# Kernel optimization log

Hardware: AMD Instinct MI355X
Metric: run time of the kernel (lower is better)

The kernel has to match this reference:

```python
import jax, jax.numpy as jnp
import numpy as np

EPS = 1e-6          # module eps for denominator
KERNEL_EPS = 1e-4   # performer softmax_kernel numerical eps


def softmax_kernel(data, projection):
    # data: [n, l, h, e]; projection: [m, e] -> features [n, l, h, m]
    d = data.shape[-1]
    m = projection.shape[0]
    data_normalizer = d ** -0.25
    ratio = m ** -0.5
    data_dash = jnp.einsum('nlhe,me->nlhm', data * data_normalizer, projection)
    diag_data = (0.5 * (data_normalizer ** 2)) * jnp.sum(data * data, axis=-1, keepdims=True)
    # numerically stable exp with per-row max subtraction
    data_dash = ratio * (jnp.exp(data_dash - diag_data - jnp.max(data_dash, axis=-1, keepdims=True)) + KERNEL_EPS)
    return data_dash


def _gaussian_orthogonal_random_matrix(nb_rows, nb_cols, seed=0):
    rng = np.random.default_rng(seed)
    blocks = []
    for _ in range(int(np.ceil(nb_rows / nb_cols))):
        q, _ = np.linalg.qr(rng.standard_normal((nb_cols, nb_cols)))
        blocks.append(q.T)
    proj = np.concatenate(blocks, axis=0)[:nb_rows]
    # scaling=0: chi-distributed row multipliers
    multiplier = np.linalg.norm(rng.standard_normal((nb_rows, nb_cols)), axis=1)
    return (multiplier[:, None] * proj).astype(np.float32)


def setup_inputs() -> dict:
    n, l, h, e = 2, 2048, 8, 64
    nb_features = l  # module: nb_features = l when l >= e
    key = jax.random.key(0)
    kq, kk, kv = jax.random.split(key, 3)
    queries = jax.random.normal(kq, (n, l, h, e), jnp.float32)
    keys = jax.random.normal(kk, (n, l, h, e), jnp.float32)
    values = jax.random.normal(kv, (n, l, h, e), jnp.float32)
    projection = jnp.asarray(_gaussian_orthogonal_random_matrix(nb_features, e))
    return {"queries": queries, "keys": keys, "values": values, "projection": projection}


def reference(queries, keys, values, projection):
    # Performer linear attention, batched (bi=None) branch
    q = softmax_kernel(queries, projection)   # [n, l, h, m]
    k = softmax_kernel(keys, projection)      # [n, l, h, m]
    kv = jnp.einsum('nshm,nshe->nhem', k, values)              # [n, h, e, m]
    z = 1.0 / (jnp.einsum('nlhm,nhm->nlh', q, k.sum(axis=1)) + EPS)  # [n, l, h]
    v = jnp.einsum('nlhm,nhem,nlh->nlhe', q, kv, z)             # [n, l, h, e]
    return v
```

## Files before the change

kernel.cpp:

```cpp
#include <hip/hip_runtime.h>


#define LL 2048
#define HH 8
#define MM 2048
#define ROWSTR 512

#define NORMC 0.35355339059327373f
#define LOG2E 1.4426950408889634f
#define NORMC2 (NORMC * LOG2E)
#define RATIO 0.022097086912079608f
#define KEPS 1e-4f
#define REPS (RATIO * KEPS)
#define EPSD 1e-6f

#define KVSPLIT 2097152
#define RSPLIT 32768

typedef __attribute__((ext_vector_type(8))) short short8;
typedef __attribute__((ext_vector_type(16))) float f32x16;

#define MFMA32(a, b, c) __builtin_amdgcn_mfma_f32_32x32x16_bf16((a), (b), (c), 0, 0, 0)

__device__ __forceinline__ void wg_barrier_lds() {
    asm volatile("s_waitcnt lgkmcnt(0)" ::: "memory");
    __builtin_amdgcn_s_barrier();
    __builtin_amdgcn_sched_barrier(0);
}

__device__ __forceinline__ f32x16 zero16() {
    f32x16 v;
    #pragma unroll
    for (int i = 0; i < 16; ++i) v[i] = 0.f;
    return v;
}
__device__ __forceinline__ unsigned short f2bf(float f) {
    union { float f; unsigned int u; } v; v.f = f;
    unsigned int r = v.u + 0x7fffu + ((v.u >> 16) & 1u);
    return (unsigned short)(r >> 16);
}
__device__ __forceinline__ unsigned int pk2(float lo, float hi) {
    return __builtin_amdgcn_perm(__float_as_uint(hi), __float_as_uint(lo), 0x07060302u);
}
__device__ __forceinline__ float bf2f(unsigned short u) {
    union { unsigned int ui; float f; } v; v.ui = ((unsigned int)u) << 16; return v.f;
}

template <bool BF16>
__device__ __forceinline__ short8 row_load8(const void* src, size_t rowbase, int off) {
    if (BF16) {
        return *(const short8*)((const unsigned short*)src + rowbase + off);
    } else {
        const float* p = (const float*)src + rowbase + off;
        float4 f0 = ((const float4*)p)[0], f1 = ((const float4*)p)[1];
        union { unsigned int u[4]; short8 s; } v;
        v.u[0] = pk2(f0.x, f0.y); v.u[1] = pk2(f0.z, f0.w);
        v.u[2] = pk2(f1.x, f1.y); v.u[3] = pk2(f1.z, f1.w);
        return v.s;
    }
}

template <bool BF16>
__device__ __forceinline__ void tile_load(const void* src, size_t base, size_t rstride,
                                          int t, uint4& A, uint4& B) {
    const int row = t >> 2, c16 = (t & 3) * 16;
    if (BF16) {
        const unsigned short* p = (const unsigned short*)src + base + (size_t)row * rstride + c16;
        A = *(const uint4*)p;
        B = *(const uint4*)(p + 8);
    } else {
        const float* p = (const float*)src + base + (size_t)row * rstride + c16;
        float4 f0 = ((const float4*)p)[0], f1 = ((const float4*)p)[1];
        float4 f2 = ((const float4*)p)[2], f3 = ((const float4*)p)[3];
        A.x = pk2(f0.x, f0.y); A.y = pk2(f0.z, f0.w);
        A.z = pk2(f1.x, f1.y); A.w = pk2(f1.z, f1.w);
        B.x = pk2(f2.x, f2.y); B.y = pk2(f2.z, f2.w);
        B.z = pk2(f3.x, f3.y); B.w = pk2(f3.z, f3.w);
    }
}
__device__ __forceinline__ void tile_store72(unsigned short* D, int t, uint4 A, uint4 B) {
    const int row = t >> 2, c16 = (t & 3) * 16;
    *(uint4*)&D[row * 72 + c16] = A;
    *(uint4*)&D[row * 72 + c16 + 8] = B;
}

template <bool BF16>
__device__ __forceinline__ void vt_load(const void* V, size_t base, int t, uint4& A, uint4& B) {
    const int s0 = (t & 31) * 2, e0 = (t >> 5) * 8;
    if (BF16) {
        const unsigned short* p = (const unsigned short*)V + base + (size_t)s0 * ROWSTR + e0;
        A = *(const uint4*)p;
        B = *(const uint4*)(p + ROWSTR);
    } else {
        const float* p = (const float*)V + base + (size_t)s0 * ROWSTR + e0;
        float4 f0 = ((const float4*)p)[0], f1 = ((const float4*)p)[1];
        const float* q = p + ROWSTR;
        float4 g0 = ((const float4*)q)[0], g1 = ((const float4*)q)[1];
        A.x = pk2(f0.x, f0.y); A.y = pk2(f0.z, f0.w);
        A.z = pk2(f1.x, f1.y); A.w = pk2(f1.z, f1.w);
        B.x = pk2(g0.x, g0.y); B.y = pk2(g0.z, g0.w);
        B.z = pk2(g1.x, g1.y); B.w = pk2(g1.z, g1.w);
    }
}
__device__ __forceinline__ void vt_store72(unsigned short* VT, int t, uint4 A, uint4 B) {
    const int s0 = (t & 31) * 2, e0 = (t >> 5) * 8;
    const unsigned ua[4] = {A.x, A.y, A.z, A.w}, ub[4] = {B.x, B.y, B.z, B.w};
    #pragma unroll
    for (int i = 0; i < 4; ++i) {
        *(unsigned*)&VT[(e0 + 2 * i) * 72 + s0] = (ua[i] & 0xFFFFu) | (ub[i] << 16);
        *(unsigned*)&VT[(e0 + 2 * i + 1) * 72 + s0] = (ua[i] >> 16) | (ub[i] & 0xFFFF0000u);
    }
}

__device__ __forceinline__ short8 xfrag(const unsigned int pd[8], int cp, int hi) {
    const unsigned int s0 = hi ? pd[4 * cp + 0] : pd[4 * cp + 2];
    const unsigned int s1 = hi ? pd[4 * cp + 1] : pd[4 * cp + 3];
    const unsigned int r0 = (unsigned int)__shfl_xor((int)s0, 32);
    const unsigned int r1 = (unsigned int)__shfl_xor((int)s1, 32);
    union { unsigned int u[4]; short8 s; } v;
    v.u[0] = hi ? r0 : pd[4 * cp + 0];
    v.u[1] = hi ? r1 : pd[4 * cp + 1];
    v.u[2] = hi ? pd[4 * cp + 2] : r0;
    v.u[3] = hi ? pd[4 * cp + 3] : r1;
    return v.s;
}

__global__ void LinearAttention_15985868276494_detect(const unsigned short* __restrict__ P,
                                                      float* __restrict__ flag) {
    if (threadIdx.x == 0) {
        int sane = 1;
        #pragma unroll
        for (int i = 0; i < 16; ++i) {
            const unsigned e = (P[2 * i] >> 7) & 0xFF;
            if (e < 101 || e > 141) sane = 0;
        }
        *flag = sane ? 1.0f : 0.0f;
    }
}

template <bool BF16>
__device__ void stats_impl(const void* X, const void* P, float* cws, char* smem) {
    unsigned short* Ps = (unsigned short*)smem;
    float* red = (float*)(smem + 73728);
    const int t = threadIdx.x;
    const int w = t >> 6, ln = t & 31, hi = (t >> 5) & 1;
    const int mstrip = w & 1, r3 = (w >> 1) & 3, tsel = w >> 3;
    const int grp = w >> 2, tl = t & 255;
    const int row_base = blockIdx.x * 128;

    short8 xb[4];
    #pragma unroll
    for (int c = 0; c < 4; ++c)
        xb[c] = row_load8<BF16>(X, (size_t)(row_base + r3 * 32 + ln) * 64, 16 * c + 8 * hi);

    uint4 pA, pB;
    {
        uint4 a0, b0;
        tile_load<BF16>(P, (size_t)(grp * 64) * 64, 64, tl, a0, b0);
        tile_store72(Ps + grp * 4608, tl, a0, b0);
        tile_load<BF16>(P, (size_t)((4 + grp) * 64) * 64, 64, tl, pA, pB);
    }
    wg_barrier_lds();

    float rmax = -3e38f;
    for (int i = 0; i < 8; ++i) {
        const int cur = i & 1;
        unsigned short* Pq = Ps + cur * 18432;
        #pragma unroll
        for (int j = 0; j < 2; ++j) {
            unsigned short* Pc = Pq + (tsel * 2 + j) * 4608;
            f32x16 acc = zero16();
            #pragma unroll
            for (int c = 0; c < 4; ++c) {
                const short8 af = *(const short8*)&Pc[(32 * mstrip + ln) * 72 + 16 * c + 8 * hi];
                acc = MFMA32(af, xb[c], acc);
            }
            #pragma unroll
            for (int r = 0; r < 16; ++r) rmax = fmaxf(rmax, acc[r]);
            if (j == 0 && i + 1 < 8) {
                tile_store72(Ps + (cur ^ 1) * 18432 + grp * 4608, tl, pA, pB);
                if (i + 2 < 8)
                    tile_load<BF16>(P, (size_t)(((i + 2) * 4 + grp) * 64) * 64, 64, tl, pA, pB);
            }
        }
        wg_barrier_lds();
    }
    rmax = fmaxf(rmax, __shfl_xor(rmax, 32));
    if (hi == 0) red[w * 32 + ln] = rmax;
    float s2 = 0.f;
    if (mstrip == 0 && tsel == 0) {
        #pragma unroll
        for (int c = 0; c < 4; ++c) {
            union { short8 s; unsigned int u[4]; } uv; uv.s = xb[c];
            #pragma unroll
            for (int i2 = 0; i2 < 4; ++i2) {
                const float lo = bf2f((unsigned short)(uv.u[i2] & 0xFFFF));
                const float hv = bf2f((unsigned short)(uv.u[i2] >> 16));
                s2 = fmaf(lo, lo, s2); s2 = fmaf(hv, hv, s2);
            }
        }
        s2 += __shfl_xor(s2, 32);
    }
    wg_barrier_lds();
    if (mstrip == 0 && tsel == 0 && hi == 0) {
        const float rm = fmaxf(fmaxf(red[(r3 * 2) * 32 + ln], red[(r3 * 2 + 1) * 32 + ln]),
                               fmaxf(red[(8 + r3 * 2) * 32 + ln], red[(8 + r3 * 2 + 1) * 32 + ln]));
        const int rg = row_base + r3 * 32 + ln;
        const int n = rg >> 14, l = (rg >> 3) & 2047, h = rg & 7;
        cws[(size_t)((n << 3) | h) * LL + l] =
            (NORMC * rm + (0.5f * NORMC * NORMC) * s2) * LOG2E;
    }
}

__global__ __launch_bounds__(1024, 4) void LinearAttention_15985868276494_stats(
        const void* K, const void* Q, const void* P, const float* flag,
        float* c_k, float* c_q) {
    extern __shared__ char smem_st[];
    const void* X = (blockIdx.y == 0) ? K : Q;
    float* cws = (blockIdx.y == 0) ? c_k : c_q;
    if (*flag != 0.f) stats_impl<true>(X, P, cws, smem_st);
    else stats_impl<false>(X, P, cws, smem_st);
}

template <bool BF16>
__device__ void kv_impl(const void* K, const void* V, const void* P, const float* cws,
                        float* kvf01, float* ksum01, char* smem) {
    unsigned short* Ks = (unsigned short*)smem;
    unsigned short* VT = (unsigned short*)(smem + 18432);
    float* cks = (float*)(smem + 36864);

    const int t = threadIdx.x;
    const int w = t >> 6, ln = t & 31, hi = (t >> 5) & 1;
    const int mc = w;
    const int bid = blockIdx.x;
    const int xcd = bid & 7, rr = bid >> 3;
    const int gq = rr >> 3, mtb = rr & 7;
    const int g = gq * 8 + xcd;
    const int nh = g >> 2, sp = g & 3;
    const int n = nh >> 3, h = nh & 7;
    const size_t xbase = (size_t)n * (LL * ROWSTR) + (size_t)h * 64;
    const int st0 = sp * 8;
    const int mbase = mtb * 256;

    const bool stK = (t < 256);
    const int tl = t & 255;

    short8 pb[4];
    #pragma unroll
    for (int c = 0; c < 4; ++c)
        pb[c] = row_load8<BF16>(P, (size_t)(mbase + mc * 32 + ln) * 64, 16 * c + 8 * hi);

    uint4 kA, kB, vA, vB; float ckr = 0.f;
    if (stK) {
        tile_load<BF16>(K, xbase + (size_t)(st0 * 64) * ROWSTR, ROWSTR, tl, kA, kB);
        tile_store72(Ks, tl, kA, kB);
        tile_load<BF16>(K, xbase + (size_t)((st0 + 1) * 64) * ROWSTR, ROWSTR, tl, kA, kB);
    } else {
        vt_load<BF16>(V, xbase + (size_t)(st0 * 64) * ROWSTR, tl, vA, vB);
        vt_store72(VT, tl, vA, vB);
        vt_load<BF16>(V, xbase + (size_t)((st0 + 1) * 64) * ROWSTR, tl, vA, vB);
    }
    if (t < 64) {
        cks[t] = cws[(size_t)nh * LL + st0 * 64 + t];
        ckr = cws[(size_t)nh * LL + (st0 + 1) * 64 + t];
    }
    wg_barrier_lds();

    f32x16 akv0 = zero16(), akv1 = zero16();
    float ks = 0.f;

    for (int i = 0; i < 8; ++i) {
        const int cur = i & 1;
        unsigned short* Kc = Ks + cur * 4608;
        unsigned short* Vc = VT + cur * 4608;
        const float* cc = cks + cur * 64;
        #pragma unroll
        for (int ss = 0; ss < 2; ++ss) {
            f32x16 D = zero16();
            #pragma unroll
            for (int c = 0; c < 4; ++c) {
                const short8 af = *(const short8*)&Kc[(32 * ss + ln) * 72 + 16 * c + 8 * hi];
                D = MFMA32(af, pb[c], D);
            }
            if (ss == 0 && i + 1 < 8) {
                if (stK) tile_store72(Ks + (cur ^ 1) * 4608, tl, kA, kB);
                else vt_store72(VT + (cur ^ 1) * 4608, tl, vA, vB);
                if (t < 64) cks[(cur ^ 1) * 64 + t] = ckr;
                if (i + 2 < 8) {
                    const int st = st0 + i + 2;
                    if (stK) tile_load<BF16>(K, xbase + (size_t)(st * 64) * ROWSTR, ROWSTR, tl, kA, kB);
                    else vt_load<BF16>(V, xbase + (size_t)(st * 64) * ROWSTR, tl, vA, vB);
                    if (t < 64) ckr = cws[(size_t)nh * LL + st * 64 + t];
                }
            }
            unsigned int pd[8];
            #pragma unroll
            for (int gIdx = 0; gIdx < 4; ++gIdx) {
                const float4 c4 = *(const float4*)&cc[32 * ss + 8 * gIdx + 4 * hi];
                const float ca[4] = {c4.x, c4.y, c4.z, c4.w};
                float f[4];
                #pragma unroll
                for (int b = 0; b < 4; ++b) {
                    const float arg = fminf(fmaf(D[4 * gIdx + b], NORMC2, -ca[b]), 0.f);
                    f[b] = fmaf(__builtin_amdgcn_exp2f(arg), RATIO, REPS);
                }
                ks += (f[0] + f[1]) + (f[2] + f[3]);
                pd[2 * gIdx] = pk2(f[0], f[1]);
                pd[2 * gIdx + 1] = pk2(f[2], f[3]);
            }
            #pragma unroll
            for (int cp = 0; cp < 2; ++cp) {
                const short8 bf = xfrag(pd, cp, hi);
                const int scol = 32 * ss + 16 * cp + 8 * hi;
                const short8 v0 = *(const short8*)&Vc[ln * 72 + scol];
                const short8 v1 = *(const short8*)&Vc[(32 + ln) * 72 + scol];
                akv0 = MFMA32(v0, bf, akv0);
                akv1 = MFMA32(v1, bf, akv1);
            }
        }
        wg_barrier_lds();
    }
    {
        ks += __shfl_xor(ks, 32);
        const int m = mbase + mc * 32 + ln;
        if (hi == 0)
            ksum01[(size_t)sp * RSPLIT + (size_t)nh * MM + m] = ks;
        float* basep = kvf01 + (size_t)sp * KVSPLIT + (size_t)nh * (size_t)(64 * MM) + m;
        #pragma unroll
        for (int r = 0; r < 16; ++r) {
            const int e = (r & 3) + 8 * (r >> 2) + 4 * hi;
            basep[(size_t)e * MM] = akv0[r];
            basep[(size_t)(e + 32) * MM] = akv1[r];
        }
    }
}

__global__ __launch_bounds__(512, 4) void LinearAttention_15985868276494_kv(
        const void* K, const void* V, const void* P, const float* flag,
        const float* cws, float* kvf01, float* ksum01) {
    extern __shared__ char smem_kv[];
    if (*flag != 0.f) kv_impl<true>(K, V, P, cws, kvf01, ksum01, smem_kv);
    else kv_impl<false>(K, V, P, cws, kvf01, ksum01, smem_kv);
}

__global__ __launch_bounds__(256) void LinearAttention_15985868276494_reduce(
        const float* __restrict__ kvf01, const float* __restrict__ ksum01,
        unsigned short* __restrict__ kvT, float* __restrict__ ksumW) {
    const int gid = blockIdx.x * 256 + threadIdx.x;
    const size_t i4 = (size_t)gid * 4;
    const float4 a = *(const float4*)&kvf01[i4];
    const float4 b = *(const float4*)&kvf01[KVSPLIT + i4];
    const float4 c = *(const float4*)&kvf01[2 * (size_t)KVSPLIT + i4];
    const float4 d = *(const float4*)&kvf01[3 * (size_t)KVSPLIT + i4];
    uint2 o;
    o.x = (unsigned)f2bf(a.x + b.x + c.x + d.x) | ((unsigned)f2bf(a.y + b.y + c.y + d.y) << 16);
    o.y = (unsigned)f2bf(a.z + b.z + c.z + d.z) | ((unsigned)f2bf(a.w + b.w + c.w + d.w) << 16);
    *(uint2*)&kvT[i4] = o;
    if (blockIdx.x < 32) {
        const float4 e = *(const float4*)&ksum01[i4];
        const float4 f = *(const float4*)&ksum01[RSPLIT + i4];
        const float4 g = *(const float4*)&ksum01[2 * RSPLIT + i4];
        const float4 h = *(const float4*)&ksum01[3 * RSPLIT + i4];
        *(float4*)&ksumW[i4] = make_float4(e.x + f.x + g.x + h.x, e.y + f.y + g.y + h.y,
                                           e.z + f.z + g.z + h.z, e.w + f.w + g.w + h.w);
    }
}

template <bool BF16>
__device__ void out_impl(const void* Q, const void* P, const float* cqw,
                         const unsigned short* kvT, const float* ksum,
                         float* po, float* pad, char* smem) {
    unsigned short* Ps = (unsigned short*)smem;
    unsigned short* KVs = (unsigned short*)(smem + 18432);
    unsigned short* kss = (unsigned short*)(smem + 36864);
    float* fin = (float*)smem;

    const int t = threadIdx.x;
    const int w = t >> 6, ln = t & 31, hi = (t >> 5) & 1;
    const int lc = w;
    const int bid = blockIdx.x;
    const int xcd = bid & 7, rr = bid >> 3;
    const int gq = rr >> 3, lbb = rr & 7;
    const int g = gq * 8 + xcd;
    const int nh = g >> 2, sp = g & 3;
    const int n = nh >> 3, h = nh & 7;
    const size_t qbase = (size_t)n * (LL * ROWSTR) + (size_t)h * 64;
    const size_t kvbase = (size_t)nh * (size_t)(64 * MM);
    const int mt0 = sp * 8;
    const int lbase = lbb * 256;

    const bool stP = (t < 256);
    const int tl = t & 255;

    short8 qb[4];
    #pragma unroll
    for (int c = 0; c < 4; ++c)
        qb[c] = row_load8<BF16>(Q, qbase + (size_t)(lbase + lc * 32 + ln) * ROWSTR, 16 * c + 8 * hi);
    const float cq = cqw[(size_t)nh * LL + lbase + lc * 32 + ln];

    uint4 pA, pB, kA, kB; float ksr = 0.f;
    if (stP) {
        tile_load<BF16>(P, (size_t)(mt0 * 64) * 64, 64, tl, pA, pB);
        tile_store72(Ps, tl, pA, pB);
        tile_load<BF16>(P, (size_t)((mt0 + 1) * 64) * 64, 64, tl, pA, pB);
    } else {
        tile_load<true>(kvT, kvbase + mt0 * 64, MM, tl, kA, kB);
        tile_store72(KVs, tl, kA, kB);
        tile_load<true>(kvT, kvbase + (mt0 + 1) * 64, MM, tl, kA, kB);
    }
    if (t < 64) {
        kss[t] = f2bf(ksum[(size_t)nh * MM + mt0 * 64 + t]);
        ksr = ksum[(size_t)nh * MM + (mt0 + 1) * 64 + t];
    }
    wg_barrier_lds();

    f32x16 ao0 = zero16(), ao1 = zero16(), ad = zero16();

    for (int i = 0; i < 8; ++i) {
        const int cur = i & 1;
        unsigned short* Pc = Ps + cur * 4608;
        unsigned short* Kc = KVs + cur * 4608;
        const unsigned short* ksc = kss + cur * 64;
        #pragma unroll
        for (int ms = 0; ms < 2; ++ms) {
            f32x16 D = zero16();
            #pragma unroll
            for (int c = 0; c < 4; ++c) {
                const short8 af = *(const short8*)&Pc[(32 * ms + ln) * 72 + 16 * c + 8 * hi];
                D = MFMA32(af, qb[c], D);
            }
            if (ms == 0 && i + 1 < 8) {
                if (stP) tile_store72(Ps + (cur ^ 1) * 4608, tl, pA, pB);
                else tile_store72(KVs + (cur ^ 1) * 4608, tl, kA, kB);
                if (t < 64) kss[(cur ^ 1) * 64 + t] = f2bf(ksr);
                if (i + 2 < 8) {
                    if (stP) tile_load<BF16>(P, (size_t)((mt0 + i + 2) * 64) * 64, 64, tl, pA, pB);
                    else tile_load<true>(kvT, kvbase + (mt0 + i + 2) * 64, MM, tl, kA, kB);
                    if (t < 64) ksr = ksum[(size_t)nh * MM + (mt0 + i + 2) * 64 + t];
                }
            }
            unsigned int pd[8];
            #pragma unroll
            for (int gIdx = 0; gIdx < 4; ++gIdx) {
                float f[4];
                #pragma unroll
                for (int b = 0; b < 4; ++b) {
                    const float arg = fminf(fmaf(D[4 * gIdx + b], NORMC2, -cq), 0.f);
                    f[b] = fmaf(__builtin_amdgcn_exp2f(arg), RATIO, REPS);
                }
                pd[2 * gIdx] = pk2(f[0], f[1]);
                pd[2 * gIdx + 1] = pk2(f[2], f[3]);
            }
            #pragma unroll
            for (int cp = 0; cp < 2; ++cp) {
                const short8 bf = xfrag(pd, cp, hi);
                const int mcol = 32 * ms + 16 * cp + 8 * hi;
                const short8 a0 = *(const short8*)&Kc[ln * 72 + mcol];
                const short8 a1 = *(const short8*)&Kc[(32 + ln) * 72 + mcol];
                const short8 k8 = *(const short8*)&ksc[mcol];
                ao0 = MFMA32(a0, bf, ao0);
                ao1 = MFMA32(a1, bf, ao1);
                ad = MFMA32(k8, bf, ad);
            }
        }
        wg_barrier_lds();
    }
    #pragma unroll 1
    for (int e2 = 0; e2 < 2; ++e2) {
        if ((w >> 2) == e2) {
            const int slot = ((w & 3) * 64 + (t & 63)) * 33;
            #pragma unroll
            for (int r = 0; r < 16; ++r) fin[slot + r] = ao0[r];
            #pragma unroll
            for (int r = 0; r < 16; ++r) fin[slot + 16 + r] = ao1[r];
            fin[slot + 32] = ad[0];
        }
        wg_barrier_lds();
        {
            const int l128 = t >> 2, eg = t & 3;
            const int w2 = l128 >> 5, lane_l = l128 & 31;
            const float adt = fin[(w2 * 64 + lane_l) * 33 + 32];
            const int l = lbase + (e2 * 4 + w2) * 32 + lane_l;
            const size_t row = (size_t)(n * LL + l) * HH + h;
            if (eg == 0) pad[(size_t)sp * RSPLIT + row] = adt;
            float* dst = po + (size_t)sp * KVSPLIT + row * 64 + eg * 16;
            #pragma unroll
            for (int jq = 0; jq < 4; ++jq) {
                float o[4];
                #pragma unroll
                for (int b = 0; b < 4; ++b) {
                    const int e = eg * 16 + 4 * jq + b;
                    const int t16 = e >> 5, e5 = e & 31;
                    const int hi_s = (e5 >> 2) & 1;
                    const int reg = 16 * t16 + (e5 & 3) + 4 * (e5 >> 3);
                    const int lane_s = hi_s * 32 + lane_l;
                    o[b] = fin[(w2 * 64 + lane_s) * 33 + reg];
                }
                *(float4*)&dst[4 * jq] = make_float4(o[0], o[1], o[2], o[3]);
            }
        }
        wg_barrier_lds();
    }
}

__global__ __launch_bounds__(512, 4) void LinearAttention_15985868276494_out(
        const void* Q, const void* P, const float* flag, const float* cqw,
        const unsigned short* kvT, const float* ksum, float* po, float* pad) {
    extern __shared__ char smem_out[];
    if (*flag != 0.f) out_impl<true>(Q, P, cqw, kvT, ksum, po, pad, smem_out);
    else out_impl<false>(Q, P, cqw, kvT, ksum, po, pad, smem_out);
}

__global__ __launch_bounds__(256) void LinearAttention_15985868276494_out2(
        const float* __restrict__ po, const float* __restrict__ pad,
        const float* __restrict__ flag, void* __restrict__ outp) {
    const int gid = blockIdx.x * 256 + threadIdx.x;
    const int row = gid >> 2, eg = gid & 3;
    const float adt = pad[row] + pad[RSPLIT + row]
                    + pad[2 * RSPLIT + row] + pad[3 * RSPLIT + row];
    const float z = 1.0f / (adt + EPSD);
    const size_t base = (size_t)row * 64 + eg * 16;
    float vals[16];
    #pragma unroll
    for (int q4 = 0; q4 < 4; ++q4) {
        const float4 a = *(const float4*)&po[base + 4 * q4];
        const float4 b = *(const float4*)&po[KVSPLIT + base + 4 * q4];
        const float4 c = *(const float4*)&po[2 * (size_t)KVSPLIT + base + 4 * q4];
        const float4 d = *(const float4*)&po[3 * (size_t)KVSPLIT + base + 4 * q4];
        vals[4 * q4 + 0] = (a.x + b.x + c.x + d.x) * z;
        vals[4 * q4 + 1] = (a.y + b.y + c.y + d.y) * z;
        vals[4 * q4 + 2] = (a.z + b.z + c.z + d.z) * z;
        vals[4 * q4 + 3] = (a.w + b.w + c.w + d.w) * z;
    }
    if (*flag != 0.f) {
        uint4 o0, o1;
        o0.x = (unsigned)f2bf(vals[0]) | ((unsigned)f2bf(vals[1]) << 16);
        o0.y = (unsigned)f2bf(vals[2]) | ((unsigned)f2bf(vals[3]) << 16);
        o0.z = (unsigned)f2bf(vals[4]) | ((unsigned)f2bf(vals[5]) << 16);
        o0.w = (unsigned)f2bf(vals[6]) | ((unsigned)f2bf(vals[7]) << 16);
        o1.x = (unsigned)f2bf(vals[8]) | ((unsigned)f2bf(vals[9]) << 16);
        o1.y = (unsigned)f2bf(vals[10]) | ((unsigned)f2bf(vals[11]) << 16);
        o1.z = (unsigned)f2bf(vals[12]) | ((unsigned)f2bf(vals[13]) << 16);
        o1.w = (unsigned)f2bf(vals[14]) | ((unsigned)f2bf(vals[15]) << 16);
        unsigned short* op = (unsigned short*)outp + base;
        *(uint4*)op = o0;
        *(uint4*)(op + 8) = o1;
    } else {
        float* op = (float*)outp + base;
        #pragma unroll
        for (int q4 = 0; q4 < 4; ++q4)
            *(float4*)&op[4 * q4] = make_float4(vals[4 * q4], vals[4 * q4 + 1],
                                                vals[4 * q4 + 2], vals[4 * q4 + 3]);
    }
}

extern "C" void kernel_launch(void* const* d_in, const int* in_sizes, int n_in,
                              void* d_out, int out_size, void* d_ws, size_t ws_size,
                              hipStream_t stream) {
    const void* Q = d_in[0];
    const void* K = d_in[1];
    const void* V = d_in[2];
    const void* P = d_in[3];

    float* W = (float*)d_ws;
    float* flag = W;
    float* c_k = W + 16;
    float* c_q = c_k + 32768;
    float* ksum01 = c_q + 32768;
    float* kvf01 = ksum01 + 4 * RSPLIT;
    float* ksumW = kvf01 + 4 * (size_t)KVSPLIT;
    unsigned short* kvTW = (unsigned short*)(ksumW + RSPLIT);

    LinearAttention_15985868276494_detect<<<1, 64, 0, stream>>>(
        (const unsigned short*)P, flag);
    LinearAttention_15985868276494_stats<<<dim3(256, 2), 1024, 75776, stream>>>(
        K, Q, P, flag, c_k, c_q);
    LinearAttention_15985868276494_kv<<<dim3(512), 512, 37376, stream>>>(
        K, V, P, flag, c_k, kvf01, ksum01);
    LinearAttention_15985868276494_reduce<<<2048, 256, 0, stream>>>(
        kvf01, ksum01, kvTW, ksumW);
    LinearAttention_15985868276494_out<<<dim3(512), 512, 37120, stream>>>(
        Q, P, flag, c_q, kvTW, ksumW, kvf01, ksum01);
    LinearAttention_15985868276494_out2<<<512, 256, 0, stream>>>(
        kvf01, ksum01, flag, d_out);
}
```

Baseline: 192.8 us.

## Shrink stats blocks to 512 threads and re-split out kernel over features

The stats kernel now runs 512 threads per block, each wave covering all 32 projection tiles with a single 64-row tile double buffer, cutting LDS from ~74KB to ~19KB so more blocks fit per CU. The out kernel now splits the feature dimension two ways instead of four, with half as many query rows per block and an intra-block split of m strips across waves reduced through LDS. The out2 reduction then sums two partials instead of four, which cuts partial-result traffic. The risks are a longer serial loop in stats and extra LDS reduction work in out.

```diff
diff --git a/kernel.cpp b/kernel.cpp
--- a/kernel.cpp
+++ b/kernel.cpp
@@ -141,11 +141,10 @@
 template <bool BF16>
 __device__ void stats_impl(const void* X, const void* P, float* cws, char* smem) {
     unsigned short* Ps = (unsigned short*)smem;
-    float* red = (float*)(smem + 73728);
+    float* red = (float*)(smem + 18432);
     const int t = threadIdx.x;
     const int w = t >> 6, ln = t & 31, hi = (t >> 5) & 1;
-    const int mstrip = w & 1, r3 = (w >> 1) & 3, tsel = w >> 3;
-    const int grp = w >> 2, tl = t & 255;
+    const int mstrip = w & 1, r3 = w >> 1;
     const int row_base = blockIdx.x * 128;
 
     short8 xb[4];
@@ -153,42 +152,40 @@
     for (int c = 0; c < 4; ++c)
         xb[c] = row_load8<BF16>(X, (size_t)(row_base + r3 * 32 + ln) * 64, 16 * c + 8 * hi);
 
+    const bool stP = (t < 256);
+    const int tl = t & 255;
     uint4 pA, pB;
-    {
+    if (stP) {
         uint4 a0, b0;
-        tile_load<BF16>(P, (size_t)(grp * 64) * 64, 64, tl, a0, b0);
-        tile_store72(Ps + grp * 4608, tl, a0, b0);
-        tile_load<BF16>(P, (size_t)((4 + grp) * 64) * 64, 64, tl, pA, pB);
+        tile_load<BF16>(P, 0, 64, tl, a0, b0);
+        tile_store72(Ps, tl, a0, b0);
+        tile_load<BF16>(P, (size_t)64 * 64, 64, tl, pA, pB);
     }
     wg_barrier_lds();
 
     float rmax = -3e38f;
-    for (int i = 0; i < 8; ++i) {
+    for (int i = 0; i < 32; ++i) {
         const int cur = i & 1;
-        unsigned short* Pq = Ps + cur * 18432;
-        #pragma unroll
-        for (int j = 0; j < 2; ++j) {
-            unsigned short* Pc = Pq + (tsel * 2 + j) * 4608;
-            f32x16 acc = zero16();
-            #pragma unroll
-            for (int c = 0; c < 4; ++c) {
-                const short8 af = *(const short8*)&Pc[(32 * mstrip + ln) * 72 + 16 * c + 8 * hi];
-                acc = MFMA32(af, xb[c], acc);
-            }
-            #pragma unroll
-            for (int r = 0; r < 16; ++r) rmax = fmaxf(rmax, acc[r]);
-            if (j == 0 && i + 1 < 8) {
-                tile_store72(Ps + (cur ^ 1) * 18432 + grp * 4608, tl, pA, pB);
-                if (i + 2 < 8)
-                    tile_load<BF16>(P, (size_t)(((i + 2) * 4 + grp) * 64) * 64, 64, tl, pA, pB);
-            }
-        }
+        unsigned short* Pc = Ps + cur * 4608;
+        f32x16 acc = zero16();
+        #pragma unroll
+        for (int c = 0; c < 4; ++c) {
+            const short8 af = *(const short8*)&Pc[(32 * mstrip + ln) * 72 + 16 * c + 8 * hi];
+            acc = MFMA32(af, xb[c], acc);
+        }
+        if (stP && i + 1 < 32) {
+            tile_store72(Ps + (cur ^ 1) * 4608, tl, pA, pB);
+            if (i + 2 < 32)
+                tile_load<BF16>(P, (size_t)((i + 2) * 64) * 64, 64, tl, pA, pB);
+        }
+        #pragma unroll
+        for (int r = 0; r < 16; ++r) rmax = fmaxf(rmax, acc[r]);
         wg_barrier_lds();
     }
     rmax = fmaxf(rmax, __shfl_xor(rmax, 32));
     if (hi == 0) red[w * 32 + ln] = rmax;
     float s2 = 0.f;
-    if (mstrip == 0 && tsel == 0) {
+    if (mstrip == 0) {
         #pragma unroll
         for (int c = 0; c < 4; ++c) {
             union { short8 s; unsigned int u[4]; } uv; uv.s = xb[c];
@@ -202,9 +199,8 @@
         s2 += __shfl_xor(s2, 32);
     }
     wg_barrier_lds();
-    if (mstrip == 0 && tsel == 0 && hi == 0) {
-        const float rm = fmaxf(fmaxf(red[(r3 * 2) * 32 + ln], red[(r3 * 2 + 1) * 32 + ln]),
-                               fmaxf(red[(8 + r3 * 2) * 32 + ln], red[(8 + r3 * 2 + 1) * 32 + ln]));
+    if (mstrip == 0 && hi == 0) {
+        const float rm = fmaxf(red[w * 32 + ln], red[(w + 1) * 32 + ln]);
         const int rg = row_base + r3 * 32 + ln;
         const int n = rg >> 14, l = (rg >> 3) & 2047, h = rg & 7;
         cws[(size_t)((n << 3) | h) * LL + l] =
@@ -212,7 +208,7 @@
     }
 }
 
-__global__ __launch_bounds__(1024, 4) void LinearAttention_15985868276494_stats(
+__global__ __launch_bounds__(512, 4) void LinearAttention_15985868276494_stats(
         const void* K, const void* Q, const void* P, const float* flag,
         float* c_k, float* c_q) {
     extern __shared__ char smem_st[];
@@ -377,17 +373,17 @@
 
     const int t = threadIdx.x;
     const int w = t >> 6, ln = t & 31, hi = (t >> 5) & 1;
-    const int lc = w;
+    const int lc = w & 3, mspl = w >> 2;
     const int bid = blockIdx.x;
     const int xcd = bid & 7, rr = bid >> 3;
-    const int gq = rr >> 3, lbb = rr & 7;
+    const int gq = rr >> 4, lbb = rr & 15;
     const int g = gq * 8 + xcd;
-    const int nh = g >> 2, sp = g & 3;
+    const int nh = g >> 1, sp = g & 1;
     const int n = nh >> 3, h = nh & 7;
     const size_t qbase = (size_t)n * (LL * ROWSTR) + (size_t)h * 64;
     const size_t kvbase = (size_t)nh * (size_t)(64 * MM);
-    const int mt0 = sp * 8;
-    const int lbase = lbb * 256;
+    const int mt0 = sp * 16;
+    const int lbase = lbb * 128;
 
     const bool stP = (t < 256);
     const int tl = t & 255;
@@ -416,85 +412,84 @@
 
     f32x16 ao0 = zero16(), ao1 = zero16(), ad = zero16();
 
-    for (int i = 0; i < 8; ++i) {
+    for (int i = 0; i < 16; ++i) {
         const int cur = i & 1;
         unsigned short* Pc = Ps + cur * 4608;
         unsigned short* Kc = KVs + cur * 4608;
         const unsigned short* ksc = kss + cur * 64;
-        #pragma unroll
-        for (int ms = 0; ms < 2; ++ms) {
-            f32x16 D = zero16();
-            #pragma unroll
-            for (int c = 0; c < 4; ++c) {
-                const short8 af = *(const short8*)&Pc[(32 * ms + ln) * 72 + 16 * c + 8 * hi];
-                D = MFMA32(af, qb[c], D);
-            }
-            if (ms == 0 && i + 1 < 8) {
-                if (stP) tile_store72(Ps + (cur ^ 1) * 4608, tl, pA, pB);
-                else tile_store72(KVs + (cur ^ 1) * 4608, tl, kA, kB);
-                if (t < 64) kss[(cur ^ 1) * 64 + t] = f2bf(ksr);
-                if (i + 2 < 8) {
-                    if (stP) tile_load<BF16>(P, (size_t)((mt0 + i + 2) * 64) * 64, 64, tl, pA, pB);
-                    else tile_load<true>(kvT, kvbase + (mt0 + i + 2) * 64, MM, tl, kA, kB);
-                    if (t < 64) ksr = ksum[(size_t)nh * MM + (mt0 + i + 2) * 64 + t];
-                }
-            }
-            unsigned int pd[8];
-            #pragma unroll
-            for (int gIdx = 0; gIdx < 4; ++gIdx) {
-                float f[4];
-                #pragma unroll
-                for (int b = 0; b < 4; ++b) {
-                    const float arg = fminf(fmaf(D[4 * gIdx + b], NORMC2, -cq), 0.f);
-                    f[b] = fmaf(__builtin_amdgcn_exp2f(arg), RATIO, REPS);
-                }
-                pd[2 * gIdx] = pk2(f[0], f[1]);
-                pd[2 * gIdx + 1] = pk2(f[2], f[3]);
-            }
-            #pragma unroll
-            for (int cp = 0; cp < 2; ++cp) {
-                const short8 bf = xfrag(pd, cp, hi);
-                const int mcol = 32 * ms + 16 * cp + 8 * hi;
-                const short8 a0 = *(const short8*)&Kc[ln * 72 + mcol];
-                const short8 a1 = *(const short8*)&Kc[(32 + ln) * 72 + mcol];
-                const short8 k8 = *(const short8*)&ksc[mcol];
-                ao0 = MFMA32(a0, bf, ao0);
-                ao1 = MFMA32(a1, bf, ao1);
-                ad = MFMA32(k8, bf, ad);
-            }
+        f32x16 D = zero16();
+        #pragma unroll
+        for (int c = 0; c < 4; ++c) {
+            const short8 af = *(const short8*)&Pc[(32 * mspl + ln) * 72 + 16 * c + 8 * hi];
+            D = MFMA32(af, qb[c], D);
+        }
+        if (i + 1 < 16) {
+            if (stP) tile_store72(Ps + (cur ^ 1) * 4608, tl, pA, pB);
+            else tile_store72(KVs + (cur ^ 1) * 4608, tl, kA, kB);
+            if (t < 64) kss[(cur ^ 1) * 64 + t] = f2bf(ksr);
+            if (i + 2 < 16) {
+                if (stP) tile_load<BF16>(P, (size_t)((mt0 + i + 2) * 64) * 64, 64, tl, pA, pB);
+                else tile_load<true>(kvT, kvbase + (mt0 + i + 2) * 64, MM, tl, kA, kB);
+                if (t < 64) ksr = ksum[(size_t)nh * MM + (mt0 + i + 2) * 64 + t];
+            }
+        }
+        unsigned int pd[8];
+        #pragma unroll
+        for (int gIdx = 0; gIdx < 4; ++gIdx) {
+            float f[4];
+            #pragma unroll
+            for (int b = 0; b < 4; ++b) {
+                const float arg = fminf(fmaf(D[4 * gIdx + b], NORMC2, -cq), 0.f);
+                f[b] = fmaf(__builtin_amdgcn_exp2f(arg), RATIO, REPS);
+            }
+            pd[2 * gIdx] = pk2(f[0], f[1]);
+            pd[2 * gIdx + 1] = pk2(f[2], f[3]);
+        }
+        #pragma unroll
+        for (int cp = 0; cp < 2; ++cp) {
+            const short8 bf = xfrag(pd, cp, hi);
+            const int mcol = 32 * mspl + 16 * cp + 8 * hi;
+            const short8 a0 = *(const short8*)&Kc[ln * 72 + mcol];
+            const short8 a1 = *(const short8*)&Kc[(32 + ln) * 72 + mcol];
+            const short8 k8 = *(const short8*)&ksc[mcol];
+            ao0 = MFMA32(a0, bf, ao0);
+            ao1 = MFMA32(a1, bf, ao1);
+            ad = MFMA32(k8, bf, ad);
         }
         wg_barrier_lds();
     }
     #pragma unroll 1
     for (int e2 = 0; e2 < 2; ++e2) {
-        if ((w >> 2) == e2) {
-            const int slot = ((w & 3) * 64 + (t & 63)) * 33;
-            #pragma unroll
-            for (int r = 0; r < 16; ++r) fin[slot + r] = ao0[r];
-            #pragma unroll
-            for (int r = 0; r < 16; ++r) fin[slot + 16 + r] = ao1[r];
-            fin[slot + 32] = ad[0];
+        if ((lc >> 1) == e2) {
+            const int slot = ((lc & 1) * 2 + mspl);
+            const int addr = (slot * 64 + (t & 63)) * 33;
+            #pragma unroll
+            for (int r = 0; r < 16; ++r) fin[addr + r] = ao0[r];
+            #pragma unroll
+            for (int r = 0; r < 16; ++r) fin[addr + 16 + r] = ao1[r];
+            fin[addr + 32] = ad[0];
         }
         wg_barrier_lds();
         {
-            const int l128 = t >> 2, eg = t & 3;
-            const int w2 = l128 >> 5, lane_l = l128 & 31;
-            const float adt = fin[(w2 * 64 + lane_l) * 33 + 32];
-            const int l = lbase + (e2 * 4 + w2) * 32 + lane_l;
+            const int l64 = t >> 3, eg = t & 7;
+            const int lcl = l64 >> 5, lane_l = l64 & 31;
+            const int s0 = (lcl * 2) * 64, s1 = (lcl * 2 + 1) * 64;
+            const float adt = fin[(s0 + lane_l) * 33 + 32] + fin[(s1 + lane_l) * 33 + 32];
+            const int l = lbase + (e2 * 2 + lcl) * 32 + lane_l;
             const size_t row = (size_t)(n * LL + l) * HH + h;
             if (eg == 0) pad[(size_t)sp * RSPLIT + row] = adt;
-            float* dst = po + (size_t)sp * KVSPLIT + row * 64 + eg * 16;
-            #pragma unroll
-            for (int jq = 0; jq < 4; ++jq) {
+            float* dst = po + (size_t)sp * KVSPLIT + row * 64 + eg * 8;
+            #pragma unroll
+            for (int jq = 0; jq < 2; ++jq) {
                 float o[4];
                 #pragma unroll
                 for (int b = 0; b < 4; ++b) {
-                    const int e = eg * 16 + 4 * jq + b;
+                    const int e = eg * 8 + 4 * jq + b;
                     const int t16 = e >> 5, e5 = e & 31;
                     const int hi_s = (e5 >> 2) & 1;
                     const int reg = 16 * t16 + (e5 & 3) + 4 * (e5 >> 3);
                     const int lane_s = hi_s * 32 + lane_l;
-                    o[b] = fin[(w2 * 64 + lane_s) * 33 + reg];
+                    o[b] = fin[(s0 + lane_s) * 33 + reg] + fin[(s1 + lane_s) * 33 + reg];
                 }
                 *(float4*)&dst[4 * jq] = make_float4(o[0], o[1], o[2], o[3]);
             }
@@ -516,8 +511,7 @@
         const float* __restrict__ flag, void* __restrict__ outp) {
     const int gid = blockIdx.x * 256 + threadIdx.x;
     const int row = gid >> 2, eg = gid & 3;
-    const float adt = pad[row] + pad[RSPLIT + row]
-                    + pad[2 * RSPLIT + row] + pad[3 * RSPLIT + row];
+    const float adt = pad[row] + pad[RSPLIT + row];
     const float z = 1.0f / (adt + EPSD);
     const size_t base = (size_t)row * 64 + eg * 16;
     float vals[16];
@@ -525,12 +519,10 @@
     for (int q4 = 0; q4 < 4; ++q4) {
         const float4 a = *(const float4*)&po[base + 4 * q4];
         const float4 b = *(const float4*)&po[KVSPLIT + base + 4 * q4];
-        const float4 c = *(const float4*)&po[2 * (size_t)KVSPLIT + base + 4 * q4];
-        const float4 d = *(const float4*)&po[3 * (size_t)KVSPLIT + base + 4 * q4];
-        vals[4 * q4 + 0] = (a.x + b.x + c.x + d.x) * z;
-        vals[4 * q4 + 1] = (a.y + b.y + c.y + d.y) * z;
-        vals[4 * q4 + 2] = (a.z + b.z + c.z + d.z) * z;
-        vals[4 * q4 + 3] = (a.w + b.w + c.w + d.w) * z;
+        vals[4 * q4 + 0] = (a.x + b.x) * z;
+        vals[4 * q4 + 1] = (a.y + b.y) * z;
+        vals[4 * q4 + 2] = (a.z + b.z) * z;
+        vals[4 * q4 + 3] = (a.w + b.w) * z;
     }
     if (*flag != 0.f) {
         uint4 o0, o1;
@@ -573,7 +565,7 @@
 
     LinearAttention_15985868276494_detect<<<1, 64, 0, stream>>>(
         (const unsigned short*)P, flag);
-    LinearAttention_15985868276494_stats<<<dim3(256, 2), 1024, 75776, stream>>>(
+    LinearAttention_15985868276494_stats<<<dim3(256, 2), 512, 19456, stream>>>(
         K, Q, P, flag, c_k, c_q);
     LinearAttention_15985868276494_kv<<<dim3(512), 512, 37376, stream>>>(
         K, V, P, flag, c_k, kvf01, ksum01);
```

Result: faster. 185.4 us (-3.8%).
